# Performance work log

Hardware: AMD Instinct MI355X
Metric: run time of the kernel (lower is better)

## Reference

```python
import jax, jax.numpy as jnp
import numpy as np
import math

B, T, M, C = 4, 2048, 16, 256   # batch, seq, m chunks, c_s chunk width
DIM = 1024                       # layer width; k = DIM // C = 4
D = 64                           # conditioning bottleneck
N_ITERS, TAU = 20, 1.0


def _diag_bias(rows, cols):
    b = np.full((rows, cols), -8.0, dtype=np.float32)
    for i in range(min(rows, cols)):
        b[i, i] = 0.0
    return jnp.asarray(b)


def setup_inputs() -> dict:
    key = jax.random.key(0)
    ks = jax.random.split(key, 10)
    state_dim = M * C
    k = DIM // C
    H_post = np.full((M, k), -8.0, dtype=np.float32)
    for i in range(M):
        H_post[i, i % k] = 0.0
    return {
        "s": jax.random.normal(ks[0], (B, T, M, C), jnp.float32),
        "gamma": 0.02 * jax.random.normal(ks[1], (state_dim,), jnp.float32),
        "compress": 0.02 * jax.random.normal(ks[2], (state_dim, D), jnp.float32),
        "alpha_pre": jnp.float32(0.01),
        "to_logits_pre": 0.02 * jax.random.normal(ks[3], (D, k * M), jnp.float32),
        "H_pre": _diag_bias(k, M),
        "alpha_align": jnp.float32(0.01),
        "to_logits_align": 0.02 * jax.random.normal(ks[4], (D, M * M), jnp.float32),
        "H_align": _diag_bias(M, M),
        "alpha_next": jnp.float32(0.01),
        "to_logits_next": 0.02 * jax.random.normal(ks[5], (D, M * M), jnp.float32),
        "H_next": _diag_bias(M, M),
        "alpha_post": jnp.float32(0.01),
        "to_logits_post": 0.02 * jax.random.normal(ks[6], (D, M * k), jnp.float32),
        "H_post": jnp.asarray(H_post),
        "W_layer": jax.random.normal(ks[7], (DIM, DIM), jnp.float32) / math.sqrt(DIM),
    }


def sinkhorn_log(logits, num_iters=N_ITERS, tau=TAU):
    """Log-domain Sinkhorn; output row-scaled so row sums = 1 * rows-normalized."""
    rows, cols = logits.shape[-2], logits.shape[-1]
    Z = logits / tau
    lr = -math.log(rows)
    lc = -math.log(cols)
    u0 = jnp.zeros(Z.shape[:-1], Z.dtype)
    v0 = jnp.zeros(Z.shape[:-2] + (cols,), Z.dtype)

    def body(_, uv):
        u, v = uv
        u = lr - jax.nn.logsumexp(Z + v[..., None, :], axis=-1)
        v = lc - jax.nn.logsumexp(Z + u[..., None], axis=-2)
        return (u, v)

    u, v = jax.lax.fori_loop(0, num_iters, body, (u0, v0))
    return jnp.exp(Z + u[..., None] + v[..., None, :]) * rows


def _route(code, alpha, to_logits, bias, state, rows, cols):
    """Fused: Sinkhorn(alpha*(code@to_logits)+bias) @ state."""
    raw = (code @ to_logits).reshape(code.shape[:-1] + (rows, cols))
    P = sinkhorn_log(alpha * raw + bias)
    return jnp.einsum('...ij,...jc->...ic', P, state)


def reference(s, gamma, compress, alpha_pre, to_logits_pre, H_pre,
              alpha_align, to_logits_align, H_align,
              alpha_next, to_logits_next, H_next,
              alpha_post, to_logits_post, H_post, W_layer):
    b, t, m, c = s.shape
    state_dim = m * c
    k = W_layer.shape[0] // c
    # RMSNorm over flattened state: F.normalize * sqrt(dim) * (gamma + 1)
    s_vec = s.reshape(b, t, state_dim)
    l2 = jnp.sqrt(jnp.sum(s_vec * s_vec, axis=-1, keepdims=True))
    s_norm = s_vec / jnp.maximum(l2, 1e-12) * jnp.sqrt(jnp.float32(state_dim)) * (gamma + 1.0)
    code = s_norm @ compress  # (b, t, d)
    # read: H_pre (k x m) routes state -> layer input
    layer_in = _route(code, alpha_pre, to_logits_pre, H_pre, s, k, m).reshape(b, t, k * c)
    layer_out = layer_in @ W_layer  # the wrapped layer_fn (dense linear)
    # write: align, absorb output via H_post, prepare next via H_next
    s_aligned = _route(code, alpha_align, to_logits_align, H_align, s, m, m)
    out_flat = layer_out.reshape(b, t, k, c)
    s_updated = s_aligned + _route(code, alpha_post, to_logits_post, H_post, out_flat, m, k)
    s_next = _route(code, alpha_next, to_logits_next, H_next, s_updated, m, m)
    return s_next
```

## Files before the change

### kernel.cpp

```cpp
#include <hip/hip_runtime.h>
#include <math.h>

#define NTOK 8192
#define SD   4096
#define ITERS 20

typedef __attribute__((ext_vector_type(8))) short short8;
typedef __attribute__((ext_vector_type(8))) unsigned short ushort8;
typedef __attribute__((ext_vector_type(4))) unsigned short us4;
typedef __attribute__((ext_vector_type(4))) float f32x4;

__device__ inline unsigned short f2bf(float x) {
    unsigned int u = __float_as_uint(x);
    unsigned int r = (u + 0x7FFFu + ((u >> 16) & 1u)) >> 16;
    return (unsigned short)r;
}
__device__ inline float bf2f(unsigned short u) {
    return __uint_as_float((unsigned int)u << 16);
}

__global__ __launch_bounds__(256) void k_preall(const float* __restrict__ W, unsigned short* __restrict__ WT,
                                                const float* __restrict__ compress, const float* __restrict__ gamma,
                                                unsigned short* __restrict__ cgT,
                                                const float* __restrict__ tl_pre, const float* __restrict__ tl_al,
                                                const float* __restrict__ tl_nx,  const float* __restrict__ tl_po,
                                                unsigned short* __restrict__ tlT)
{
    const int b = blockIdx.x;
    const int tid = threadIdx.x;
    if (b < 256) {
        __shared__ float tb[64][65];
        const int k0 = (b >> 4) * 64, n0 = (b & 15) * 64;
        #pragma unroll 4
        for (int q = 0; q < 16; ++q) {
            const int idx = q * 256 + tid;
            const int r = idx >> 6, c = idx & 63;
            tb[r][c] = W[(size_t)(k0 + r) * 1024 + n0 + c];
        }
        __syncthreads();
        #pragma unroll 4
        for (int q = 0; q < 16; ++q) {
            const int idx = q * 256 + tid;
            const int n = idx >> 6, k = idx & 63;
            WT[(size_t)(n0 + n) * 1024 + k0 + k] = f2bf(tb[k][n]);
        }
    } else if (b < 320) {
        __shared__ float tb2[64][65];
        __shared__ float gsh[64];
        const int k0 = (b - 256) * 64;
        #pragma unroll 4
        for (int q = 0; q < 16; ++q) {
            const int idx = q * 256 + tid;
            const int r = idx >> 6, dd = idx & 63;
            tb2[r][dd] = compress[(size_t)(k0 + r) * 64 + dd];
        }
        if (tid < 64) gsh[tid] = gamma[k0 + tid] + 1.0f;
        __syncthreads();
        #pragma unroll 4
        for (int q = 0; q < 16; ++q) {
            const int idx = q * 256 + tid;
            const int d = idx >> 6, r = idx & 63;
            cgT[(size_t)d * SD + k0 + r] = f2bf(tb2[r][d] * gsh[r]);
        }
    } else {
        const int idx = (b - 320) * 256 + tid;
        const int k = idx / 640, n = idx - k * 640;
        float v;
        if (n < 64)       v = tl_pre[k * 64 + n];
        else if (n < 320) v = tl_al[k * 256 + (n - 64)];
        else if (n < 576) v = tl_nx[k * 256 + (n - 320)];
        else              v = tl_po[k * 64 + (n - 576)];
        tlT[(size_t)n * 64 + k] = f2bf(v);
    }
}

__global__ __launch_bounds__(256) void k_front(const float* __restrict__ s,
                                               const unsigned short* __restrict__ cgT,
                                               const unsigned short* __restrict__ tlT,
                                               const float* __restrict__ a_pre_p, const float* __restrict__ H_pre,
                                               const float* __restrict__ a_al_p,  const float* __restrict__ H_al,
                                               const float* __restrict__ a_nx_p,  const float* __restrict__ H_nx,
                                               const float* __restrict__ a_po_p,  const float* __restrict__ H_po,
                                               float* __restrict__ Ppre,
                                               float* __restrict__ Pna, float* __restrict__ Pnp,
                                               unsigned short* __restrict__ s_bf)
{
    __shared__ __align__(16) char smem[64320];
    unsigned short* code_sh = (unsigned short*)(smem);
    unsigned short* s_sh    = (unsigned short*)(smem + 2304);
    unsigned short* cg_sh   = (unsigned short*)(smem + 2304 + 4864);
    float*          red     = (float*)(smem + 2304);
    unsigned short* lg_sh   = (unsigned short*)(smem + 2304);
    float*          Pal_sh  = (float*)(smem + 26624);
    float*          Pnx_sh  = (float*)(smem + 43264);
    float*          Ppo_sh  = (float*)(smem + 59904);
    float*          ssq_sh  = (float*)(smem + 64256);

    const int tid  = threadIdx.x;
    const int lane = tid & 63;
    const int wid  = tid >> 6;
    const int tok0 = blockIdx.x * 16;
    const int st_tok = tid >> 4;
    const int st_k   = (tid & 15) * 8;
    const int sg_d   = tid >> 2;
    const int sg_k   = (tid & 3) * 32;
    const int wk = wid * 32;

    float ssq = 0.f;
    f32x4 acc[4];
    #pragma unroll
    for (int ni = 0; ni < 4; ++ni) acc[ni] = (f32x4){0.f, 0.f, 0.f, 0.f};

    for (int ks = 0; ks < 32; ++ks) {
        const int kg = ks * 128;
        __syncthreads();
        {
            const float4* sp = (const float4*)(s + (size_t)(tok0 + st_tok) * SD + kg + st_k);
            float4 v0 = sp[0], v1 = sp[1];
            ssq += v0.x*v0.x + v0.y*v0.y + v0.z*v0.z + v0.w*v0.w
                 + v1.x*v1.x + v1.y*v1.y + v1.z*v1.z + v1.w*v1.w;
            ushort8 pk;
            pk[0]=f2bf(v0.x); pk[1]=f2bf(v0.y); pk[2]=f2bf(v0.z); pk[3]=f2bf(v0.w);
            pk[4]=f2bf(v1.x); pk[5]=f2bf(v1.y); pk[6]=f2bf(v1.z); pk[7]=f2bf(v1.w);
            *(ushort8*)(s_sh + st_tok * 152 + st_k) = pk;
            if (s_bf)
                *(ushort8*)(s_bf + (size_t)(tok0 + st_tok) * SD + kg + st_k) = pk;
        }
        {
            const ushort8* gp = (const ushort8*)(cgT + (size_t)sg_d * SD + kg + sg_k);
            ushort8 c0 = gp[0], c1 = gp[1], c2 = gp[2], c3 = gp[3];
            ushort8* cw = (ushort8*)(cg_sh + sg_d * 152 + sg_k);
            cw[0] = c0; cw[1] = c1; cw[2] = c2; cw[3] = c3;
        }
        __syncthreads();

        short8 a = *(const short8*)(s_sh + (lane & 15) * 152 + wk + (lane >> 4) * 8);
        short8 b[4];
        #pragma unroll
        for (int ni = 0; ni < 4; ++ni)
            b[ni] = *(const short8*)(cg_sh + (ni * 16 + (lane & 15)) * 152 + wk + (lane >> 4) * 8);
        #pragma unroll
        for (int ni = 0; ni < 4; ++ni)
            acc[ni] = __builtin_amdgcn_mfma_f32_16x16x32_bf16(a, b[ni], acc[ni], 0, 0, 0);
    }

    ssq += __shfl_xor(ssq, 1);
    ssq += __shfl_xor(ssq, 2);
    ssq += __shfl_xor(ssq, 4);
    ssq += __shfl_xor(ssq, 8);
    __syncthreads();
    if ((tid & 15) == 0) ssq_sh[st_tok] = ssq;

    #pragma unroll
    for (int ni = 0; ni < 4; ++ni)
        #pragma unroll
        for (int r = 0; r < 4; ++r)
            red[wid * 1088 + ((lane >> 4) * 4 + r) * 68 + ni * 16 + (lane & 15)] = acc[ni][r];
    __syncthreads();
    if (tid < 16) ssq_sh[tid] = 64.0f / fmaxf(sqrtf(ssq_sh[tid]), 1e-12f);
    __syncthreads();
    #pragma unroll
    for (int q = 0; q < 4; ++q) {
        const int idx = q * 256 + tid;
        const int tok = idx >> 6, d = idx & 63;
        float v = red[0 * 1088 + tok * 68 + d] + red[1 * 1088 + tok * 68 + d]
                + red[2 * 1088 + tok * 68 + d] + red[3 * 1088 + tok * 68 + d];
        code_sh[tok * 72 + d] = f2bf(v * ssq_sh[tok]);
    }
    __syncthreads();

    {
        f32x4 acc2[10];
        #pragma unroll
        for (int ni = 0; ni < 10; ++ni) acc2[ni] = (f32x4){0.f, 0.f, 0.f, 0.f};
        const int nbase = wid * 160;
        #pragma unroll
        for (int ks = 0; ks < 2; ++ks) {
            const int ko = ks * 32 + (lane >> 4) * 8;
            short8 a = *(const short8*)(code_sh + (lane & 15) * 72 + ko);
            #pragma unroll
            for (int ni = 0; ni < 10; ++ni) {
                short8 b = *(const short8*)(tlT + (size_t)(nbase + ni * 16 + (lane & 15)) * 64 + ko);
                acc2[ni] = __builtin_amdgcn_mfma_f32_16x16x32_bf16(a, b, acc2[ni], 0, 0, 0);
            }
        }
        #pragma unroll
        for (int ni = 0; ni < 10; ++ni)
            #pragma unroll
            for (int r = 0; r < 4; ++r)
                lg_sh[((lane >> 4) * 4 + r) * 656 + nbase + ni * 16 + (lane & 15)] = f2bf(acc2[ni][r]);
    }
    __syncthreads();

    const int t_in = lane >> 2;
    const int sub  = lane & 3;
    const int tok  = tok0 + t_in;

    if (wid < 2) {
        const float alpha = (wid == 0) ? (*a_al_p) : (*a_nx_p);
        const float* Hp   = ((wid == 0) ? H_al : H_nx) + sub * 64;
        const unsigned short* lgp = lg_sh + t_in * 656 + (wid == 0 ? 64 : 320) + sub * 64;
        float Km[4][16];
        #pragma unroll
        for (int rr = 0; rr < 4; ++rr)
            #pragma unroll
            for (int h = 0; h < 2; ++h) {
                ushort8 rv = *(const ushort8*)(lgp + rr * 16 + h * 8);
                float4 h0 = *(const float4*)(Hp + rr * 16 + h * 8);
                float4 h1 = *(const float4*)(Hp + rr * 16 + h * 8 + 4);
                Km[rr][h*8+0] = expf(alpha * bf2f(rv[0]) + h0.x);
                Km[rr][h*8+1] = expf(alpha * bf2f(rv[1]) + h0.y);
                Km[rr][h*8+2] = expf(alpha * bf2f(rv[2]) + h0.z);
                Km[rr][h*8+3] = expf(alpha * bf2f(rv[3]) + h0.w);
                Km[rr][h*8+4] = expf(alpha * bf2f(rv[4]) + h1.x);
                Km[rr][h*8+5] = expf(alpha * bf2f(rv[5]) + h1.y);
                Km[rr][h*8+6] = expf(alpha * bf2f(rv[6]) + h1.z);
                Km[rr][h*8+7] = expf(alpha * bf2f(rv[7]) + h1.w);
            }
        float v[16], u[4];
        #pragma unroll
        for (int c = 0; c < 16; ++c) v[c] = 1.0f;
        for (int it = 0; it < ITERS; ++it) {
            #pragma unroll
            for (int rr = 0; rr < 4; ++rr) {
                float su = 0.f;
                #pragma unroll
                for (int c = 0; c < 16; ++c) su += Km[rr][c] * v[c];
                u[rr] = 0.0625f * __builtin_amdgcn_rcpf(su);
            }
            float pv[16];
            #pragma unroll
            for (int c = 0; c < 16; ++c)
                pv[c] = Km[0][c]*u[0] + Km[1][c]*u[1] + Km[2][c]*u[2] + Km[3][c]*u[3];
            #pragma unroll
            for (int c = 0; c < 16; ++c) pv[c] += __shfl_xor(pv[c], 1);
            #pragma unroll
            for (int c = 0; c < 16; ++c) pv[c] += __shfl_xor(pv[c], 2);
            #pragma unroll
            for (int c = 0; c < 16; ++c) v[c] = 0.0625f * __builtin_amdgcn_rcpf(pv[c]);
        }
        float* dst = ((wid == 0) ? Pal_sh : Pnx_sh) + t_in * 260;
        #pragma unroll
        for (int rr = 0; rr < 4; ++rr) {
            const float su16 = 16.0f * u[rr];
            #pragma unroll
            for (int c = 0; c < 16; ++c)
                dst[(sub * 4 + rr) * 16 + c] = Km[rr][c] * su16 * v[c];
        }
    } else if (wid == 2) {
        const float alpha = *a_pre_p;
        const unsigned short* lgp = lg_sh + t_in * 656 + sub * 16;
        const float* Hp  = H_pre + sub * 16;
        float Km[16];
        #pragma unroll
        for (int h = 0; h < 2; ++h) {
            ushort8 rv = *(const ushort8*)(lgp + h * 8);
            float4 h0 = *(const float4*)(Hp + h * 8);
            float4 h1 = *(const float4*)(Hp + h * 8 + 4);
            Km[h*8+0] = expf(alpha * bf2f(rv[0]) + h0.x);
            Km[h*8+1] = expf(alpha * bf2f(rv[1]) + h0.y);
            Km[h*8+2] = expf(alpha * bf2f(rv[2]) + h0.z);
            Km[h*8+3] = expf(alpha * bf2f(rv[3]) + h0.w);
            Km[h*8+4] = expf(alpha * bf2f(rv[4]) + h1.x);
            Km[h*8+5] = expf(alpha * bf2f(rv[5]) + h1.y);
            Km[h*8+6] = expf(alpha * bf2f(rv[6]) + h1.z);
            Km[h*8+7] = expf(alpha * bf2f(rv[7]) + h1.w);
        }
        float v[16], u;
        #pragma unroll
        for (int c = 0; c < 16; ++c) v[c] = 1.0f;
        for (int it = 0; it < ITERS; ++it) {
            float su = 0.f;
            #pragma unroll
            for (int c = 0; c < 16; ++c) su += Km[c] * v[c];
            u = 0.25f * __builtin_amdgcn_rcpf(su);
            float pv[16];
            #pragma unroll
            for (int c = 0; c < 16; ++c) pv[c] = Km[c] * u;
            #pragma unroll
            for (int c = 0; c < 16; ++c) pv[c] += __shfl_xor(pv[c], 1);
            #pragma unroll
            for (int c = 0; c < 16; ++c) pv[c] += __shfl_xor(pv[c], 2);
            #pragma unroll
            for (int c = 0; c < 16; ++c) v[c] = 0.0625f * __builtin_amdgcn_rcpf(pv[c]);
        }
        const float su4 = 4.0f * u;
        #pragma unroll
        for (int c = 0; c < 16; ++c)
            Ppre[(size_t)tok * 64 + sub * 16 + c] = Km[c] * su4 * v[c];
    } else {
        const float alpha = *a_po_p;
        const unsigned short* lgp = lg_sh + t_in * 656 + 576 + sub * 16;
        const float* Hp  = H_po + sub * 16;
        float Km[4][4];
        #pragma unroll
        for (int rr = 0; rr < 4; ++rr) {
            us4 rv = *(const us4*)(lgp + rr * 4);
            float4 hv = *(const float4*)(Hp + rr * 4);
            Km[rr][0] = expf(alpha * bf2f(rv[0]) + hv.x);
            Km[rr][1] = expf(alpha * bf2f(rv[1]) + hv.y);
            Km[rr][2] = expf(alpha * bf2f(rv[2]) + hv.z);
            Km[rr][3] = expf(alpha * bf2f(rv[3]) + hv.w);
        }
        float v[4], u[4];
        #pragma unroll
        for (int c = 0; c < 4; ++c) v[c] = 1.0f;
        for (int it = 0; it < ITERS; ++it) {
            #pragma unroll
            for (int rr = 0; rr < 4; ++rr) {
                float su = 0.f;
                #pragma unroll
                for (int c = 0; c < 4; ++c) su += Km[rr][c] * v[c];
                u[rr] = 0.0625f * __builtin_amdgcn_rcpf(su);
            }
            float pv[4];
            #pragma unroll
            for (int c = 0; c < 4; ++c)
                pv[c] = Km[0][c]*u[0] + Km[1][c]*u[1] + Km[2][c]*u[2] + Km[3][c]*u[3];
            #pragma unroll
            for (int c = 0; c < 4; ++c) pv[c] += __shfl_xor(pv[c], 1);
            #pragma unroll
            for (int c = 0; c < 4; ++c) pv[c] += __shfl_xor(pv[c], 2);
            #pragma unroll
            for (int c = 0; c < 4; ++c) v[c] = 0.25f * __builtin_amdgcn_rcpf(pv[c]);
        }
        #pragma unroll
        for (int rr = 0; rr < 4; ++rr) {
            const float su16 = 16.0f * u[rr];
            #pragma unroll
            for (int c = 0; c < 4; ++c)
                Ppo_sh[t_in * 68 + (sub * 4 + rr) * 4 + c] = Km[rr][c] * su16 * v[c];
        }
    }
    __syncthreads();

    const int ct = tid >> 4;
    const int cj = tid & 15;
    const float* pnx = Pnx_sh + ct * 260;
    const float* pal = Pal_sh + ct * 260;
    const float* ppo = Ppo_sh + ct * 68;
    #pragma unroll
    for (int m = 0; m < 16; ++m) {
        float a2 = 0.f;
        #pragma unroll
        for (int t2 = 0; t2 < 16; ++t2) a2 += pnx[m * 16 + t2] * pal[t2 * 16 + cj];
        Pna[(size_t)(tok0 + ct) * 256 + m * 16 + cj] = a2;
    }
    #pragma unroll
    for (int e = 0; e < 4; ++e) {
        const int idx = cj * 4 + e;
        const int m = idx >> 2, q = idx & 3;
        float a2 = 0.f;
        #pragma unroll
        for (int t2 = 0; t2 < 16; ++t2) a2 += pnx[m * 16 + t2] * ppo[t2 * 4 + q];
        Pnp[(size_t)(tok0 + ct) * 64 + idx] = a2;
    }
}

template<bool SBF>
__global__ __launch_bounds__(256) void k_apply2(const float* __restrict__ s,
                                                const unsigned short* __restrict__ s_bf,
                                                const float* __restrict__ Ppre,
                                                unsigned short* __restrict__ layer_in)
{
    __shared__ float s_sh[SD];
    __shared__ float P_sh[64];
    const int tid = threadIdx.x;
    const int tok = blockIdx.x;

    if (SBF) {
        #pragma unroll
        for (int c2 = 0; c2 < 2; ++c2) {
            ushort8 v = *(const ushort8*)(s_bf + (size_t)tok * SD + c2 * 2048 + tid * 8);
            float4 f0, f1;
            f0.x = bf2f(v[0]); f0.y = bf2f(v[1]); f0.z = bf2f(v[2]); f0.w = bf2f(v[3]);
            f1.x = bf2f(v[4]); f1.y = bf2f(v[5]); f1.z = bf2f(v[6]); f1.w = bf2f(v[7]);
            *(float4*)(s_sh + c2 * 2048 + tid * 8)     = f0;
            *(float4*)(s_sh + c2 * 2048 + tid * 8 + 4) = f1;
        }
    } else {
        const float4* sp4 = (const float4*)(s + (size_t)tok * SD);
        #pragma unroll
        for (int j = 0; j < 4; ++j)
            *(float4*)(s_sh + j * 1024 + tid * 4) = sp4[j * 256 + tid];
    }
    if (tid < 64) P_sh[tid] = Ppre[(size_t)tok * 64 + tid];
    __syncthreads();

    #pragma unroll
    for (int i = 0; i < 4; ++i) {
        float acc = 0.f;
        #pragma unroll
        for (int j = 0; j < 16; ++j) acc += P_sh[i * 16 + j] * s_sh[j * 256 + tid];
        layer_in[(size_t)tok * 1024 + i * 256 + tid] = f2bf(acc);
    }
}

__global__ __launch_bounds__(256) void k_gemm_bf16(const unsigned short* __restrict__ A,
                                                   const unsigned short* __restrict__ BT,
                                                   unsigned short* __restrict__ Cb)
{
    __shared__ unsigned short Abuf[128 * 48];
    __shared__ unsigned short Bbuf[128 * 48];
    const int tid  = threadIdx.x;
    const int lane = tid & 63;
    const int wid  = tid >> 6;
    const int wr   = wid >> 1, wc = wid & 1;
    const int m0 = blockIdx.y * 128, n0 = blockIdx.x * 128;

    f32x4 acc[4][4];
    #pragma unroll
    for (int mi = 0; mi < 4; ++mi)
        #pragma unroll
        for (int ni = 0; ni < 4; ++ni) acc[mi][ni] = (f32x4){0.f, 0.f, 0.f, 0.f};

    for (int k0 = 0; k0 < 1024; k0 += 32) {
        __syncthreads();
        #pragma unroll
        for (int h = 0; h < 2; ++h) {
            const int idx = h * 256 + tid;
            const int row = idx >> 2, kq = idx & 3;
            float4 av = *(const float4*)(A + (size_t)(m0 + row) * 1024 + k0 + kq * 8);
            *(float4*)(Abuf + row * 48 + kq * 8) = av;
            float4 bv = *(const float4*)(BT + (size_t)(n0 + row) * 1024 + k0 + kq * 8);
            *(float4*)(Bbuf + row * 48 + kq * 8) = bv;
        }
        __syncthreads();

        short8 a[4], b[4];
        #pragma unroll
        for (int mi = 0; mi < 4; ++mi)
            a[mi] = *(const short8*)(Abuf + (wr * 64 + mi * 16 + (lane & 15)) * 48 + (lane >> 4) * 8);
        #pragma unroll
        for (int ni = 0; ni < 4; ++ni)
            b[ni] = *(const short8*)(Bbuf + (wc * 64 + ni * 16 + (lane & 15)) * 48 + (lane >> 4) * 8);
        #pragma unroll
        for (int mi = 0; mi < 4; ++mi)
            #pragma unroll
            for (int ni = 0; ni < 4; ++ni)
                acc[mi][ni] = __builtin_amdgcn_mfma_f32_16x16x32_bf16(a[mi], b[ni], acc[mi][ni], 0, 0, 0);
    }

    #pragma unroll
    for (int mi = 0; mi < 4; ++mi)
        #pragma unroll
        for (int ni = 0; ni < 4; ++ni)
            #pragma unroll
            for (int r = 0; r < 4; ++r)
                Cb[(size_t)(m0 + wr * 64 + mi * 16 + (lane >> 4) * 4 + r) * 1024 +
                   n0 + wc * 64 + ni * 16 + (lane & 15)] = f2bf(acc[mi][ni][r]);
}

template<bool SBF>
__global__ __launch_bounds__(256) void k_final2(const float* __restrict__ s,
                                                const unsigned short* __restrict__ s_bf,
                                                const unsigned short* __restrict__ lo_bf,
                                                const float* __restrict__ Pna,
                                                const float* __restrict__ Pnp,
                                                float* __restrict__ out)
{
    __shared__ float s_sh[SD];
    __shared__ float lo_sh[1024];
    __shared__ float Pna_sh[256];
    __shared__ float Pnp_sh[64];
    const int tid = threadIdx.x;
    const int tok = blockIdx.x;

    if (SBF) {
        #pragma unroll
        for (int c2 = 0; c2 < 2; ++c2) {
            ushort8 v = *(const ushort8*)(s_bf + (size_t)tok * SD + c2 * 2048 + tid * 8);
            float4 f0, f1;
            f0.x = bf2f(v[0]); f0.y = bf2f(v[1]); f0.z = bf2f(v[2]); f0.w = bf2f(v[3]);
            f1.x = bf2f(v[4]); f1.y = bf2f(v[5]); f1.z = bf2f(v[6]); f1.w = bf2f(v[7]);
            *(float4*)(s_sh + c2 * 2048 + tid * 8)     = f0;
            *(float4*)(s_sh + c2 * 2048 + tid * 8 + 4) = f1;
        }
    } else {
        const float4* sp4 = (const float4*)(s + (size_t)tok * SD);
        #pragma unroll
        for (int j = 0; j < 4; ++j)
            *(float4*)(s_sh + j * 1024 + tid * 4) = sp4[j * 256 + tid];
    }
    {
        us4 lv = *(const us4*)(lo_bf + (size_t)tok * 1024 + tid * 4);
        float4 f;
        f.x = bf2f(lv[0]); f.y = bf2f(lv[1]); f.z = bf2f(lv[2]); f.w = bf2f(lv[3]);
        *(float4*)(lo_sh + tid * 4) = f;
    }
    Pna_sh[tid] = Pna[(size_t)tok * 256 + tid];
    if (tid < 64) Pnp_sh[tid] = Pnp[(size_t)tok * 64 + tid];
    __syncthreads();

    const int c = tid;
    #pragma unroll
    for (int m = 0; m < 16; ++m) {
        float acc = 0.f;
        #pragma unroll
        for (int j = 0; j < 16; ++j) acc += Pna_sh[m * 16 + j] * s_sh[j * 256 + c];
        #pragma unroll
        for (int q = 0; q < 4; ++q) acc += Pnp_sh[m * 4 + q] * lo_sh[q * 256 + c];
        out[(size_t)tok * SD + m * 256 + c] = acc;
    }
}

extern "C" void kernel_launch(void* const* d_in, const int* in_sizes, int n_in,
                              void* d_out, int out_size, void* d_ws, size_t ws_size,
                              hipStream_t stream)
{
    const float* s        = (const float*)d_in[0];
    const float* gamma    = (const float*)d_in[1];
    const float* compress = (const float*)d_in[2];
    const float* a_pre    = (const float*)d_in[3];
    const float* tl_pre   = (const float*)d_in[4];
    const float* H_pre    = (const float*)d_in[5];
    const float* a_al     = (const float*)d_in[6];
    const float* tl_al    = (const float*)d_in[7];
    const float* H_al     = (const float*)d_in[8];
    const float* a_nx     = (const float*)d_in[9];
    const float* tl_nx    = (const float*)d_in[10];
    const float* H_nx     = (const float*)d_in[11];
    const float* a_po     = (const float*)d_in[12];
    const float* tl_po    = (const float*)d_in[13];
    const float* H_po     = (const float*)d_in[14];
    const float* W        = (const float*)d_in[15];
    float* out = (float*)d_out;

    char* p = (char*)d_ws;
    unsigned short* lo_bf    = (unsigned short*)p; p += (size_t)8192 * 1024 * 2;
    float* Pna               = (float*)p;          p += (size_t)8192 * 256 * 4;
    float* Pnp               = (float*)p;          p += (size_t)8192 * 64 * 4;
    unsigned short* layer_in = (unsigned short*)p; p += (size_t)8192 * 1024 * 2;
    unsigned short* WT       = (unsigned short*)p; p += (size_t)1024 * 1024 * 2;
    unsigned short* cgT      = (unsigned short*)p; p += (size_t)64 * SD * 2;
    unsigned short* tlT      = (unsigned short*)p; p += (size_t)640 * 64 * 2 + 128;
    float* Ppre              = (float*)p;          p += (size_t)8192 * 64 * 4;
    unsigned short* s_bf     = (unsigned short*)p; p += (size_t)NTOK * SD * 2;
    const bool use_sbf = ((size_t)(p - (char*)d_ws) <= ws_size);

    k_preall<<<480, 256, 0, stream>>>(W, WT, compress, gamma, cgT,
                                      tl_pre, tl_al, tl_nx, tl_po, tlT);
    k_front<<<512, 256, 0, stream>>>(s, cgT, tlT,
                                     a_pre, H_pre, a_al, H_al,
                                     a_nx, H_nx, a_po, H_po,
                                     Ppre, Pna, Pnp,
                                     use_sbf ? s_bf : (unsigned short*)nullptr);
    if (use_sbf) {
        k_apply2<true><<<NTOK, 256, 0, stream>>>(s, s_bf, Ppre, layer_in);
    } else {
        k_apply2<false><<<NTOK, 256, 0, stream>>>(s, s_bf, Ppre, layer_in);
    }
    k_gemm_bf16<<<dim3(8, 64), 256, 0, stream>>>(layer_in, WT, lo_bf);
    if (use_sbf) {
        k_final2<true><<<NTOK, 256, 0, stream>>>(s, s_bf, lo_bf, Pna, Pnp, out);
    } else {
        k_final2<false><<<NTOK, 256, 0, stream>>>(s, s_bf, lo_bf, Pna, Pnp, out);
    }
}
```

Baseline: 195.9 us.

## Drop bf16 state copy, load MFMA operands directly from global in front kernel

```diff
diff --git a/kernel.cpp b/kernel.cpp
--- a/kernel.cpp
+++ b/kernel.cpp
@@ -74,82 +74,65 @@
     }
 }
 
-__global__ __launch_bounds__(256) void k_front(const float* __restrict__ s,
-                                               const unsigned short* __restrict__ cgT,
-                                               const unsigned short* __restrict__ tlT,
-                                               const float* __restrict__ a_pre_p, const float* __restrict__ H_pre,
-                                               const float* __restrict__ a_al_p,  const float* __restrict__ H_al,
-                                               const float* __restrict__ a_nx_p,  const float* __restrict__ H_nx,
-                                               const float* __restrict__ a_po_p,  const float* __restrict__ H_po,
-                                               float* __restrict__ Ppre,
-                                               float* __restrict__ Pna, float* __restrict__ Pnp,
-                                               unsigned short* __restrict__ s_bf)
+#define LGS 660
+__global__ __launch_bounds__(256) void k_front2(const float* __restrict__ s,
+                                                const unsigned short* __restrict__ cgT,
+                                                const unsigned short* __restrict__ tlT,
+                                                const float* __restrict__ a_pre_p, const float* __restrict__ H_pre,
+                                                const float* __restrict__ a_al_p,  const float* __restrict__ H_al,
+                                                const float* __restrict__ a_nx_p,  const float* __restrict__ H_nx,
+                                                const float* __restrict__ a_po_p,  const float* __restrict__ H_po,
+                                                float* __restrict__ Ppre,
+                                                float* __restrict__ Pna, float* __restrict__ Pnp)
 {
-    __shared__ __align__(16) char smem[64320];
-    unsigned short* code_sh = (unsigned short*)(smem);
-    unsigned short* s_sh    = (unsigned short*)(smem + 2304);
-    unsigned short* cg_sh   = (unsigned short*)(smem + 2304 + 4864);
-    float*          red     = (float*)(smem + 2304);
-    unsigned short* lg_sh   = (unsigned short*)(smem + 2304);
-    float*          Pal_sh  = (float*)(smem + 26624);
-    float*          Pnx_sh  = (float*)(smem + 43264);
-    float*          Ppo_sh  = (float*)(smem + 59904);
-    float*          ssq_sh  = (float*)(smem + 64256);
+    __shared__ __align__(16) char smem[61440];
+    unsigned short* code_sh  = (unsigned short*)(smem);
+    float*          red      = (float*)(smem + 2304);
+    unsigned short* lg_sh    = (unsigned short*)(smem + 2304);
+    float*          Pal_sh   = (float*)(smem + 23424);
+    float*          Pnx_sh   = (float*)(smem + 40064);
+    float*          Ppo_sh   = (float*)(smem + 56704);
+    float*          ssq_part = (float*)(smem + 61056);
+    float*          ssq_sh   = (float*)(smem + 61312);
 
     const int tid  = threadIdx.x;
     const int lane = tid & 63;
     const int wid  = tid >> 6;
     const int tok0 = blockIdx.x * 16;
-    const int st_tok = tid >> 4;
-    const int st_k   = (tid & 15) * 8;
-    const int sg_d   = tid >> 2;
-    const int sg_k   = (tid & 3) * 32;
-    const int wk = wid * 32;
+    const int row  = lane & 15;
+    const int kq   = lane >> 4;
+    const int wk   = wid * 32;
 
     float ssq = 0.f;
     f32x4 acc[4];
     #pragma unroll
     for (int ni = 0; ni < 4; ++ni) acc[ni] = (f32x4){0.f, 0.f, 0.f, 0.f};
 
+    const float*          srow  = s   + (size_t)(tok0 + row) * SD + wk + kq * 8;
+    const unsigned short* cgrow = cgT + wk + kq * 8;
+
+    #pragma unroll 2
     for (int ks = 0; ks < 32; ++ks) {
         const int kg = ks * 128;
-        __syncthreads();
-        {
-            const float4* sp = (const float4*)(s + (size_t)(tok0 + st_tok) * SD + kg + st_k);
-            float4 v0 = sp[0], v1 = sp[1];
-            ssq += v0.x*v0.x + v0.y*v0.y + v0.z*v0.z + v0.w*v0.w
-                 + v1.x*v1.x + v1.y*v1.y + v1.z*v1.z + v1.w*v1.w;
-            ushort8 pk;
-            pk[0]=f2bf(v0.x); pk[1]=f2bf(v0.y); pk[2]=f2bf(v0.z); pk[3]=f2bf(v0.w);
-            pk[4]=f2bf(v1.x); pk[5]=f2bf(v1.y); pk[6]=f2bf(v1.z); pk[7]=f2bf(v1.w);
-            *(ushort8*)(s_sh + st_tok * 152 + st_k) = pk;
-            if (s_bf)
-                *(ushort8*)(s_bf + (size_t)(tok0 + st_tok) * SD + kg + st_k) = pk;
-        }
-        {
-            const ushort8* gp = (const ushort8*)(cgT + (size_t)sg_d * SD + kg + sg_k);
-            ushort8 c0 = gp[0], c1 = gp[1], c2 = gp[2], c3 = gp[3];
-            ushort8* cw = (ushort8*)(cg_sh + sg_d * 152 + sg_k);
-            cw[0] = c0; cw[1] = c1; cw[2] = c2; cw[3] = c3;
-        }
-        __syncthreads();
-
-        short8 a = *(const short8*)(s_sh + (lane & 15) * 152 + wk + (lane >> 4) * 8);
+        float4 v0 = *(const float4*)(srow + kg);
+        float4 v1 = *(const float4*)(srow + kg + 4);
+        ssq += v0.x*v0.x + v0.y*v0.y + v0.z*v0.z + v0.w*v0.w
+             + v1.x*v1.x + v1.y*v1.y + v1.z*v1.z + v1.w*v1.w;
+        short8 a;
+        a[0]=(short)f2bf(v0.x); a[1]=(short)f2bf(v0.y); a[2]=(short)f2bf(v0.z); a[3]=(short)f2bf(v0.w);
+        a[4]=(short)f2bf(v1.x); a[5]=(short)f2bf(v1.y); a[6]=(short)f2bf(v1.z); a[7]=(short)f2bf(v1.w);
         short8 b[4];
         #pragma unroll
         for (int ni = 0; ni < 4; ++ni)
-            b[ni] = *(const short8*)(cg_sh + (ni * 16 + (lane & 15)) * 152 + wk + (lane >> 4) * 8);
+            b[ni] = *(const short8*)(cgrow + (size_t)(ni * 16 + row) * SD + kg);
         #pragma unroll
         for (int ni = 0; ni < 4; ++ni)
             acc[ni] = __builtin_amdgcn_mfma_f32_16x16x32_bf16(a, b[ni], acc[ni], 0, 0, 0);
     }
 
-    ssq += __shfl_xor(ssq, 1);
-    ssq += __shfl_xor(ssq, 2);
-    ssq += __shfl_xor(ssq, 4);
-    ssq += __shfl_xor(ssq, 8);
-    __syncthreads();
-    if ((tid & 15) == 0) ssq_sh[st_tok] = ssq;
+    ssq += __shfl_xor(ssq, 16);
+    ssq += __shfl_xor(ssq, 32);
+    if (lane < 16) ssq_part[wid * 16 + row] = ssq;
 
     #pragma unroll
     for (int ni = 0; ni < 4; ++ni)
@@ -157,7 +140,10 @@
         for (int r = 0; r < 4; ++r)
             red[wid * 1088 + ((lane >> 4) * 4 + r) * 68 + ni * 16 + (lane & 15)] = acc[ni][r];
     __syncthreads();
-    if (tid < 16) ssq_sh[tid] = 64.0f / fmaxf(sqrtf(ssq_sh[tid]), 1e-12f);
+    if (tid < 16) {
+        float t = ssq_part[tid] + ssq_part[16 + tid] + ssq_part[32 + tid] + ssq_part[48 + tid];
+        ssq_sh[tid] = 64.0f / fmaxf(sqrtf(t), 1e-12f);
+    }
     __syncthreads();
     #pragma unroll
     for (int q = 0; q < 4; ++q) {
@@ -188,7 +174,7 @@
         for (int ni = 0; ni < 10; ++ni)
             #pragma unroll
             for (int r = 0; r < 4; ++r)
-                lg_sh[((lane >> 4) * 4 + r) * 656 + nbase + ni * 16 + (lane & 15)] = f2bf(acc2[ni][r]);
+                lg_sh[((lane >> 4) * 4 + r) * LGS + nbase + ni * 16 + (lane & 15)] = f2bf(acc2[ni][r]);
     }
     __syncthreads();
 
@@ -199,7 +185,7 @@
     if (wid < 2) {
         const float alpha = (wid == 0) ? (*a_al_p) : (*a_nx_p);
         const float* Hp   = ((wid == 0) ? H_al : H_nx) + sub * 64;
-        const unsigned short* lgp = lg_sh + t_in * 656 + (wid == 0 ? 64 : 320) + sub * 64;
+        const unsigned short* lgp = lg_sh + t_in * LGS + (wid == 0 ? 64 : 320) + sub * 64;
         float Km[4][16];
         #pragma unroll
         for (int rr = 0; rr < 4; ++rr)
@@ -249,7 +235,7 @@
         }
     } else if (wid == 2) {
         const float alpha = *a_pre_p;
-        const unsigned short* lgp = lg_sh + t_in * 656 + sub * 16;
+        const unsigned short* lgp = lg_sh + t_in * LGS + sub * 16;
         const float* Hp  = H_pre + sub * 16;
         float Km[16];
         #pragma unroll
@@ -290,7 +276,7 @@
             Ppre[(size_t)tok * 64 + sub * 16 + c] = Km[c] * su4 * v[c];
     } else {
         const float alpha = *a_po_p;
-        const unsigned short* lgp = lg_sh + t_in * 656 + 576 + sub * 16;
+        const unsigned short* lgp = lg_sh + t_in * LGS + 576 + sub * 16;
         const float* Hp  = H_po + sub * 16;
         float Km[4][4];
         #pragma unroll
@@ -357,28 +343,16 @@
     }
 }
 
-template<bool SBF>
-__global__ __launch_bounds__(256) void k_apply2(const float* __restrict__ s,
-                                                const unsigned short* __restrict__ s_bf,
-                                                const float* __restrict__ Ppre,
-                                                unsigned short* __restrict__ layer_in)
+__global__ __launch_bounds__(256) void k_apply(const float* __restrict__ s,
+                                               const float* __restrict__ Ppre,
+                                               unsigned short* __restrict__ layer_in)
 {
     __shared__ float s_sh[SD];
     __shared__ float P_sh[64];
     const int tid = threadIdx.x;
     const int tok = blockIdx.x;
 
-    if (SBF) {
-        #pragma unroll
-        for (int c2 = 0; c2 < 2; ++c2) {
-            ushort8 v = *(const ushort8*)(s_bf + (size_t)tok * SD + c2 * 2048 + tid * 8);
-            float4 f0, f1;
-            f0.x = bf2f(v[0]); f0.y = bf2f(v[1]); f0.z = bf2f(v[2]); f0.w = bf2f(v[3]);
-            f1.x = bf2f(v[4]); f1.y = bf2f(v[5]); f1.z = bf2f(v[6]); f1.w = bf2f(v[7]);
-            *(float4*)(s_sh + c2 * 2048 + tid * 8)     = f0;
-            *(float4*)(s_sh + c2 * 2048 + tid * 8 + 4) = f1;
-        }
-    } else {
+    {
         const float4* sp4 = (const float4*)(s + (size_t)tok * SD);
         #pragma unroll
         for (int j = 0; j < 4; ++j)
@@ -451,13 +425,11 @@
                    n0 + wc * 64 + ni * 16 + (lane & 15)] = f2bf(acc[mi][ni][r]);
 }
 
-template<bool SBF>
-__global__ __launch_bounds__(256) void k_final2(const float* __restrict__ s,
-                                                const unsigned short* __restrict__ s_bf,
-                                                const unsigned short* __restrict__ lo_bf,
-                                                const float* __restrict__ Pna,
-                                                const float* __restrict__ Pnp,
-                                                float* __restrict__ out)
+__global__ __launch_bounds__(256) void k_final(const float* __restrict__ s,
+                                               const unsigned short* __restrict__ lo_bf,
+                                               const float* __restrict__ Pna,
+                                               const float* __restrict__ Pnp,
+                                               float* __restrict__ out)
 {
     __shared__ float s_sh[SD];
     __shared__ float lo_sh[1024];
@@ -466,17 +438,7 @@
     const int tid = threadIdx.x;
     const int tok = blockIdx.x;
 
-    if (SBF) {
-        #pragma unroll
-        for (int c2 = 0; c2 < 2; ++c2) {
-            ushort8 v = *(const ushort8*)(s_bf + (size_t)tok * SD + c2 * 2048 + tid * 8);
-            float4 f0, f1;
-            f0.x = bf2f(v[0]); f0.y = bf2f(v[1]); f0.z = bf2f(v[2]); f0.w = bf2f(v[3]);
-            f1.x = bf2f(v[4]); f1.y = bf2f(v[5]); f1.z = bf2f(v[6]); f1.w = bf2f(v[7]);
-            *(float4*)(s_sh + c2 * 2048 + tid * 8)     = f0;
-            *(float4*)(s_sh + c2 * 2048 + tid * 8 + 4) = f1;
-        }
-    } else {
+    {
         const float4* sp4 = (const float4*)(s + (size_t)tok * SD);
         #pragma unroll
         for (int j = 0; j < 4; ++j)
@@ -535,25 +497,14 @@
     unsigned short* cgT      = (unsigned short*)p; p += (size_t)64 * SD * 2;
     unsigned short* tlT      = (unsigned short*)p; p += (size_t)640 * 64 * 2 + 128;
     float* Ppre              = (float*)p;          p += (size_t)8192 * 64 * 4;
-    unsigned short* s_bf     = (unsigned short*)p; p += (size_t)NTOK * SD * 2;
-    const bool use_sbf = ((size_t)(p - (char*)d_ws) <= ws_size);
 
     k_preall<<<480, 256, 0, stream>>>(W, WT, compress, gamma, cgT,
                                       tl_pre, tl_al, tl_nx, tl_po, tlT);
-    k_front<<<512, 256, 0, stream>>>(s, cgT, tlT,
-                                     a_pre, H_pre, a_al, H_al,
-                                     a_nx, H_nx, a_po, H_po,
-                                     Ppre, Pna, Pnp,
-                                     use_sbf ? s_bf : (unsigned short*)nullptr);
-    if (use_sbf) {
-        k_apply2<true><<<NTOK, 256, 0, stream>>>(s, s_bf, Ppre, layer_in);
-    } else {
-        k_apply2<false><<<NTOK, 256, 0, stream>>>(s, s_bf, Ppre, layer_in);
-    }
+    k_front2<<<512, 256, 0, stream>>>(s, cgT, tlT,
+                                      a_pre, H_pre, a_al, H_al,
+                                      a_nx, H_nx, a_po, H_po,
+                                      Ppre, Pna, Pnp);
+    k_apply<<<NTOK, 256, 0, stream>>>(s, Ppre, layer_in);
     k_gemm_bf16<<<dim3(8, 64), 256, 0, stream>>>(layer_in, WT, lo_bf);
-    if (use_sbf) {
-        k_final2<true><<<NTOK, 256, 0, stream>>>(s, s_bf, lo_bf, Pna, Pnp, out);
-    } else {
-        k_final2<false><<<NTOK, 256, 0, stream>>>(s, s_bf, lo_bf, Pna, Pnp, out);
-    }
-}
+    k_final<<<NTOK, 256, 0, stream>>>(s, lo_bf, Pna, Pnp, out);
+}
```

Result: no change. 195.7 us (-0.1%).
